# Performance work log

Measured on AMD Instinct MI355X. Metric: run time of the kernel, lower is better.

Reference implementation:

```python
import jax, jax.numpy as jnp
import numpy as np

B, S, D = 2, 2048, 4096
H, KV = 32, 8
HD = D // H  # 128
REP = H // KV  # 4
THETA = 10000.0


def _rope(x, cos, sin):
    # x: [B, S, N, HD]; cos/sin: [S, HD//2]
    xs = x.reshape(*x.shape[:-1], HD // 2, 2)
    x0, x1 = xs[..., 0], xs[..., 1]
    c = cos[None, :, None, :]
    s = sin[None, :, None, :]
    r0 = x0 * c - x1 * s
    r1 = x0 * s + x1 * c
    return jnp.stack([r0, r1], axis=-1).reshape(x.shape)


def setup_inputs() -> dict:
    key = jax.random.key(0)
    kx, kq, kk, kv, ko = jax.random.split(key, 5)
    x = jax.random.normal(kx, (B, S, D), dtype=jnp.float32)
    # faithful rope frequencies (precompute_freqs_cis equivalent)
    inv_freq = 1.0 / (THETA ** (np.arange(0, HD, 2, dtype=np.float32) / HD))
    freqs = np.outer(np.arange(S, dtype=np.float32), inv_freq)  # [S, HD//2]
    freqs_cos = jnp.asarray(np.cos(freqs))
    freqs_sin = jnp.asarray(np.sin(freqs))
    std = 0.02
    wq = jax.random.normal(kq, (H * HD, D), dtype=jnp.float32) * std
    wk = jax.random.normal(kk, (KV * HD, D), dtype=jnp.float32) * std
    wv = jax.random.normal(kv, (KV * HD, D), dtype=jnp.float32) * std
    wo = jax.random.normal(ko, (D, H * HD), dtype=jnp.float32) * std
    return {"x": x, "freqs_cos": freqs_cos, "freqs_sin": freqs_sin,
            "wq": wq, "wk": wk, "wv": wv, "wo": wo}


def reference(x, freqs_cos, freqs_sin, wq, wk, wv, wo):
    bs, seqlen, _ = x.shape
    q = (x @ wq.T).reshape(bs, seqlen, H, HD)
    k = (x @ wk.T).reshape(bs, seqlen, KV, HD)
    v = (x @ wv.T).reshape(bs, seqlen, KV, HD)
    q = _rope(q, freqs_cos, freqs_sin)
    k = _rope(k, freqs_cos, freqs_sin)
    # GQA: group query heads by kv head instead of materializing repeat_kv
    qg = q.reshape(bs, seqlen, KV, REP, HD)
    scale = 1.0 / jnp.sqrt(jnp.float32(HD))
    scores = jnp.einsum("bqgrd,bkgd->bgrqk", qg, k) * scale  # [B,KV,REP,S,S]
    causal = jnp.tril(jnp.ones((seqlen, seqlen), dtype=bool))
    scores = jnp.where(causal, scores, -jnp.inf)
    probs = jax.nn.softmax(scores, axis=-1)
    out = jnp.einsum("bgrqk,bkgd->bqgrd", probs, v)  # [B,S,KV,REP,HD]
    out = out.reshape(bs, seqlen, H * HD)
    return out @ wo.T
```

## Files before the change

### kernel.cpp

```cpp
#include <hip/hip_runtime.h>
#include <hip/hip_bf16.h>

#define BB 2
#define SS 2048
#define DD 4096
#define HH 32
#define KVH 8
#define HDD 128

using bf16 = __hip_bfloat16;
typedef __attribute__((ext_vector_type(8))) __bf16 bf16x8;
typedef __attribute__((ext_vector_type(4))) float f32x4;

#define GLOAD16(gp, lp) __builtin_amdgcn_global_load_lds(                     \
    (const __attribute__((address_space(1))) void*)(gp),                      \
    (__attribute__((address_space(3))) void*)(lp), 16, 0, 0)

__global__ __launch_bounds__(256) void cast_kernel(
    const float* __restrict__ s, bf16* __restrict__ d, int n4) {
  int i = blockIdx.x * blockDim.x + threadIdx.x;
  if (i >= n4) return;
  float4 v = ((const float4*)s)[i];
  bf16 a0 = __float2bfloat16(v.x), a1 = __float2bfloat16(v.y);
  bf16 a2 = __float2bfloat16(v.z), a3 = __float2bfloat16(v.w);
  ushort4 u;
  u.x = reinterpret_cast<unsigned short&>(a0);
  u.y = reinterpret_cast<unsigned short&>(a1);
  u.z = reinterpret_cast<unsigned short&>(a2);
  u.w = reinterpret_cast<unsigned short&>(a3);
  ((ushort4*)d)[i] = u;
}

__global__ __launch_bounds__(256) void rope_kernel(
    bf16* __restrict__ qb, bf16* __restrict__ kb,
    const float* __restrict__ fc, const float* __restrict__ fs) {
  int idx = blockIdx.x * blockDim.x + threadIdx.x;
  const int QP = BB * SS * HH * (HDD / 2);
  const int KP = BB * SS * KVH * (HDD / 2);
  bf16* p;
  int s, i;
  if (idx < QP) {
    int hr = idx >> 6;
    s = (hr >> 5) & (SS - 1);
    i = idx & 63;
    p = qb + ((size_t)hr << 7) + (i << 1);
  } else {
    int j = idx - QP;
    if (j >= KP) return;
    int hr = j >> 6;
    s = (hr >> 3) & (SS - 1);
    i = j & 63;
    p = kb + ((size_t)hr << 7) + (i << 1);
  }
  float c = fc[s * 64 + i], sn = fs[s * 64 + i];
  float x0 = __bfloat162float(p[0]), x1 = __bfloat162float(p[1]);
  p[0] = __float2bfloat16(x0 * c - x1 * sn);
  p[1] = __float2bfloat16(x0 * sn + x1 * c);
}

template <int MODE>
__global__ __launch_bounds__(256, 2) void gemm_bt(
    const bf16* __restrict__ A, const bf16* __restrict__ Bm,
    void* __restrict__ C, int M, int N, int K) {
  __shared__ __attribute__((aligned(16))) bf16 As[128 * 64];
  __shared__ __attribute__((aligned(16))) bf16 Bs[128 * 64];
  const int m0 = blockIdx.y * 128, n0 = blockIdx.x * 128;
  const int t = threadIdx.x;
  const int lane = t & 63, w = t >> 6;
  const int wm = (w >> 1) * 64, wn = (w & 1) * 64;
  const int lr = lane & 15, quad = lane >> 4;

  const int srow = t >> 3;
  const int scol8 = ((t & 7) ^ (srow & 7)) * 8;
  const bf16* aSrc = A + (size_t)(m0 + srow) * K + scol8;
  const bf16* bSrc = Bm + (size_t)(n0 + srow) * K + scol8;
  bf16* aDst = As + t * 8;
  bf16* bDst = Bs + t * 8;

  const int sl[2] = {((0 * 4 + quad) ^ (lr & 7)) * 8, ((1 * 4 + quad) ^ (lr & 7)) * 8};

  f32x4 acc[4][4];
#pragma unroll
  for (int i = 0; i < 4; i++)
#pragma unroll
    for (int j = 0; j < 4; j++) acc[i][j] = (f32x4)0.0f;

  for (int k0 = 0; k0 < K; k0 += 64) {
#pragma unroll
    for (int i = 0; i < 4; i++) {
      GLOAD16(aSrc + i * 32 * K, aDst + i * 2048);
      GLOAD16(bSrc + i * 32 * K, bDst + i * 2048);
    }
    __syncthreads();
#pragma unroll
    for (int kk = 0; kk < 2; kk++) {
      bf16x8 af[4], bfv[4];
#pragma unroll
      for (int i = 0; i < 4; i++)
        af[i] = *(const bf16x8*)(As + (wm + i * 16 + lr) * 64 + sl[kk]);
#pragma unroll
      for (int j = 0; j < 4; j++)
        bfv[j] = *(const bf16x8*)(Bs + (wn + j * 16 + lr) * 64 + sl[kk]);
#pragma unroll
      for (int i = 0; i < 4; i++)
#pragma unroll
        for (int j = 0; j < 4; j++)
          acc[i][j] = __builtin_amdgcn_mfma_f32_16x16x32_bf16(af[i], bfv[j], acc[i][j], 0, 0, 0);
    }
    __syncthreads();
    aSrc += 64;
    bSrc += 64;
  }

#pragma unroll
  for (int i = 0; i < 4; i++)
#pragma unroll
    for (int j = 0; j < 4; j++)
#pragma unroll
      for (int r = 0; r < 4; r++) {
        int row = m0 + wm + i * 16 + quad * 4 + r;
        int col = n0 + wn + j * 16 + lr;
        float v = acc[i][j][r];
        if (MODE == 0) {
          ((bf16*)C)[(size_t)row * N + col] = __float2bfloat16(v);
        } else if (MODE == 1) {
          ((float*)C)[(size_t)row * N + col] = v;
        } else {
          int bb = row >> 11, s = row & (SS - 1);
          int kv = col >> 7, d = col & (HDD - 1);
          ((bf16*)C)[((size_t)(bb * KVH + kv) * HDD + d) * SS + s] = __float2bfloat16(v);
        }
      }
}

__global__ __launch_bounds__(256, 2) void flash_kernel(
    const bf16* __restrict__ q, const bf16* __restrict__ k,
    const bf16* __restrict__ vt, bf16* __restrict__ out) {
  __shared__ __attribute__((aligned(16))) bf16 Ks[64 * 128];
  __shared__ __attribute__((aligned(16))) bf16 Vs[128 * 64];
  __shared__ __attribute__((aligned(16))) bf16 Ps[128 * 72];
  const int qt = gridDim.x - 1 - blockIdx.x;
  const int h = blockIdx.y, b = blockIdx.z;
  const int kv = h >> 2;
  const int t = threadIdx.x;
  const int lane = t & 63, w = t >> 6;
  const int lr = lane & 15, quad = lane >> 4;
  const int q0 = qt * 128;
  const int wr = w * 32;

  bf16x8 qf[2][4];
#pragma unroll
  for (int mf = 0; mf < 2; mf++) {
    const bf16* qp =
        q + ((size_t)(b * SS + q0 + wr + mf * 16 + lr) * HH + h) * HDD + quad * 8;
#pragma unroll
    for (int c = 0; c < 4; c++) qf[mf][c] = *(const bf16x8*)(qp + c * 32);
  }
  const float scale = 0.08838834764831845f;
#pragma unroll
  for (int mf = 0; mf < 2; mf++)
#pragma unroll
    for (int c = 0; c < 4; c++)
#pragma unroll
      for (int j = 0; j < 8; j++)
        qf[mf][c][j] = (__bf16)((float)qf[mf][c][j] * scale);

  f32x4 oa[2][8];
#pragma unroll
  for (int mf = 0; mf < 2; mf++)
#pragma unroll
    for (int i = 0; i < 8; i++) oa[mf][i] = (f32x4)0.0f;
  float m_i[8], l_i[8];
#pragma unroll
  for (int r = 0; r < 8; r++) { m_i[r] = -1e30f; l_i[r] = 0.f; }

  const int krow = t >> 4;
  const int kcol8 = ((t & 15) ^ (krow & 15)) * 8;
  const bf16* kSrc0 = k + ((size_t)(b * SS + krow) * KVH + kv) * HDD + kcol8;
  const int vrow = t >> 3;
  const int vcol8 = ((t & 7) ^ (vrow & 7)) * 8;
  const bf16* vSrc0 = vt + ((size_t)(b * KVH + kv) * HDD + vrow) * SS + vcol8;
  bf16* kDst = Ks + t * 8;
  bf16* vDst = Vs + t * 8;

  const int slV[2] = {((0 * 4 + quad) ^ (lr & 7)) * 8, ((1 * 4 + quad) ^ (lr & 7)) * 8};

  const int nkt = 2 * qt + 2;
  for (int kt = 0; kt < nkt; kt++) {
    const int kt0 = kt * 64;
    const bf16* kSrc = kSrc0 + (size_t)kt0 * (KVH * HDD);
    const bf16* vSrc = vSrc0 + kt0;
#pragma unroll
    for (int i = 0; i < 4; i++) {
      GLOAD16(kSrc + i * 16 * KVH * HDD, kDst + i * 2048);
      GLOAD16(vSrc + i * 32 * SS, vDst + i * 2048);
    }
    __syncthreads();

    f32x4 sc[2][4];
#pragma unroll
    for (int mf = 0; mf < 2; mf++)
#pragma unroll
      for (int ni = 0; ni < 4; ni++) sc[mf][ni] = (f32x4)0.0f;
#pragma unroll
    for (int c = 0; c < 4; c++) {
      bf16x8 kf[4];
#pragma unroll
      for (int ni = 0; ni < 4; ni++)
        kf[ni] = *(const bf16x8*)(Ks + (ni * 16 + lr) * 128 + (((c * 4 + quad) ^ lr) * 8));
#pragma unroll
      for (int mf = 0; mf < 2; mf++)
#pragma unroll
        for (int ni = 0; ni < 4; ni++)
          sc[mf][ni] = __builtin_amdgcn_mfma_f32_16x16x32_bf16(qf[mf][c], kf[ni], sc[mf][ni], 0, 0, 0);
    }

    if (kt0 + 63 > q0 + wr) {
#pragma unroll
      for (int mf = 0; mf < 2; mf++)
#pragma unroll
        for (int ni = 0; ni < 4; ni++)
#pragma unroll
          for (int r = 0; r < 4; r++) {
            int kidx = kt0 + ni * 16 + lr;
            int qidx = q0 + wr + mf * 16 + quad * 4 + r;
            if (kidx > qidx) sc[mf][ni][r] = -1e30f;
          }
    }

    float mx[8];
#pragma unroll
    for (int r = 0; r < 8; r++) mx[r] = -1e30f;
#pragma unroll
    for (int mf = 0; mf < 2; mf++)
#pragma unroll
      for (int ni = 0; ni < 4; ni++)
#pragma unroll
        for (int r = 0; r < 4; r++)
          mx[mf * 4 + r] = fmaxf(mx[mf * 4 + r], sc[mf][ni][r]);
#pragma unroll
    for (int off = 1; off < 16; off <<= 1)
#pragma unroll
      for (int r = 0; r < 8; r++) mx[r] = fmaxf(mx[r], __shfl_xor(mx[r], off));

    float alpha[8], rs[8];
#pragma unroll
    for (int r = 0; r < 8; r++) {
      float mn = fmaxf(m_i[r], mx[r]);
      alpha[r] = __expf(m_i[r] - mn);
      m_i[r] = mn;
      rs[r] = 0.f;
    }
#pragma unroll
    for (int mf = 0; mf < 2; mf++)
#pragma unroll
      for (int ni = 0; ni < 4; ni++)
#pragma unroll
        for (int r = 0; r < 4; r++) {
          float p = __expf(sc[mf][ni][r] - m_i[mf * 4 + r]);
          sc[mf][ni][r] = p;
          rs[mf * 4 + r] += p;
        }
#pragma unroll
    for (int off = 1; off < 16; off <<= 1)
#pragma unroll
      for (int r = 0; r < 8; r++) rs[r] += __shfl_xor(rs[r], off);
#pragma unroll
    for (int r = 0; r < 8; r++) l_i[r] = l_i[r] * alpha[r] + rs[r];
#pragma unroll
    for (int mf = 0; mf < 2; mf++)
#pragma unroll
      for (int ni = 0; ni < 8; ni++)
#pragma unroll
        for (int r = 0; r < 4; r++) oa[mf][ni][r] *= alpha[mf * 4 + r];

#pragma unroll
    for (int mf = 0; mf < 2; mf++)
#pragma unroll
      for (int ni = 0; ni < 4; ni++)
#pragma unroll
        for (int r = 0; r < 4; r++)
          Ps[(wr + mf * 16 + quad * 4 + r) * 72 + ni * 16 + lr] =
              __float2bfloat16(sc[mf][ni][r]);

#pragma unroll
    for (int kk = 0; kk < 2; kk++) {
      bf16x8 pf[2];
#pragma unroll
      for (int mf = 0; mf < 2; mf++)
        pf[mf] = *(const bf16x8*)(Ps + (wr + mf * 16 + lr) * 72 + kk * 32 + quad * 8);
#pragma unroll
      for (int ni = 0; ni < 8; ni++) {
        bf16x8 vf = *(const bf16x8*)(Vs + (ni * 16 + lr) * 64 + slV[kk]);
#pragma unroll
        for (int mf = 0; mf < 2; mf++)
          oa[mf][ni] = __builtin_amdgcn_mfma_f32_16x16x32_bf16(pf[mf], vf, oa[mf][ni], 0, 0, 0);
      }
    }
    __syncthreads();
  }

#pragma unroll
  for (int mf = 0; mf < 2; mf++)
#pragma unroll
    for (int r = 0; r < 4; r++) {
      float inv = 1.0f / l_i[mf * 4 + r];
      int srow = q0 + wr + mf * 16 + quad * 4 + r;
#pragma unroll
      for (int ni = 0; ni < 8; ni++) {
        int col = ni * 16 + lr;
        out[(size_t)(b * SS + srow) * DD + h * HDD + col] =
            __float2bfloat16(oa[mf][ni][r] * inv);
      }
    }
}

extern "C" void kernel_launch(void* const* d_in, const int* in_sizes, int n_in,
                              void* d_out, int out_size, void* d_ws, size_t ws_size,
                              hipStream_t stream) {
  (void)in_sizes; (void)n_in; (void)out_size; (void)ws_size;
  const float* x  = (const float*)d_in[0];
  const float* fc = (const float*)d_in[1];
  const float* fs = (const float*)d_in[2];
  const float* wq = (const float*)d_in[3];
  const float* wk = (const float*)d_in[4];
  const float* wv = (const float*)d_in[5];
  const float* wo = (const float*)d_in[6];

  char* ws = (char*)d_ws;
  bf16* xb   = (bf16*)(ws);
  bf16* W    = (bf16*)(ws + (size_t)33554432);
  bf16* qb   = (bf16*)(ws + (size_t)67108864);
  bf16* kb   = (bf16*)(ws + (size_t)100663296);
  bf16* vtb  = (bf16*)(ws + (size_t)109051904);
  bf16* attn = xb;

  const int NX  = BB * SS * DD;
  const int NW  = DD * DD;
  const int NWK = KVH * HDD * DD;

  cast_kernel<<<NX / 1024, 256, 0, stream>>>(x, xb, NX / 4);
  cast_kernel<<<NW / 1024, 256, 0, stream>>>(wq, W, NW / 4);
  gemm_bt<0><<<dim3(32, 32), 256, 0, stream>>>(xb, W, qb, BB * SS, DD, DD);
  cast_kernel<<<NWK / 1024, 256, 0, stream>>>(wk, W, NWK / 4);
  gemm_bt<0><<<dim3(8, 32), 256, 0, stream>>>(xb, W, kb, BB * SS, KVH * HDD, DD);
  cast_kernel<<<NWK / 1024, 256, 0, stream>>>(wv, W, NWK / 4);
  gemm_bt<2><<<dim3(8, 32), 256, 0, stream>>>(xb, W, vtb, BB * SS, KVH * HDD, DD);
  rope_kernel<<<(BB * SS * (HH + KVH) * 64) / 256, 256, 0, stream>>>(qb, kb, fc, fs);
  flash_kernel<<<dim3(SS / 128, HH, BB), 256, 0, stream>>>(qb, kb, vtb, attn);
  cast_kernel<<<NW / 1024, 256, 0, stream>>>(wo, W, NW / 4);
  gemm_bt<1><<<dim3(32, 32), 256, 0, stream>>>(attn, W, (float*)d_out, BB * SS, DD, DD);
}
```

Measured before the change: 858.5 us.

## Fuse K/V projections, fold softmax scale into RoPE, transpose score MFMA

The K and V projection GEMMs become one launch over a concatenated 2048-column weight, with the epilogue routing K columns row-major and V columns transposed. The softmax scale and log2(e) are folded into the Q RoPE pass, so the flash kernel drops its per-load Q scaling and uses exp2. The score MFMA operands are swapped so each lane holds one query row, which cuts the row max and sum reductions to two cross-lane shuffles and lets P be written to LDS as packed 8-byte stores. In exchange, the per-row alpha and l factors must be broadcast with extra shuffles, and Q is rounded to bf16 after scaling.

```diff
diff --git a/kernel.cpp b/kernel.cpp
--- a/kernel.cpp
+++ b/kernel.cpp
@@ -15,6 +15,12 @@
 #define GLOAD16(gp, lp) __builtin_amdgcn_global_load_lds(                     \
     (const __attribute__((address_space(1))) void*)(gp),                      \
     (__attribute__((address_space(3))) void*)(lp), 16, 0, 0)
+
+__device__ inline unsigned pack_bf16_2(float a, float b) {
+  unsigned short ua = __bfloat16_as_ushort(__float2bfloat16(a));
+  unsigned short ub = __bfloat16_as_ushort(__float2bfloat16(b));
+  return (unsigned)ua | ((unsigned)ub << 16);
+}
 
 __global__ __launch_bounds__(256) void cast_kernel(
     const float* __restrict__ s, bf16* __restrict__ d, int n4) {
@@ -34,16 +40,19 @@
 __global__ __launch_bounds__(256) void rope_kernel(
     bf16* __restrict__ qb, bf16* __restrict__ kb,
     const float* __restrict__ fc, const float* __restrict__ fs) {
+  const float QS = 0.08838834764831845f * 1.4426950408889634f;
   int idx = blockIdx.x * blockDim.x + threadIdx.x;
   const int QP = BB * SS * HH * (HDD / 2);
   const int KP = BB * SS * KVH * (HDD / 2);
   bf16* p;
   int s, i;
+  float g;
   if (idx < QP) {
     int hr = idx >> 6;
     s = (hr >> 5) & (SS - 1);
     i = idx & 63;
     p = qb + ((size_t)hr << 7) + (i << 1);
+    g = QS;
   } else {
     int j = idx - QP;
     if (j >= KP) return;
@@ -51,17 +60,18 @@
     s = (hr >> 3) & (SS - 1);
     i = j & 63;
     p = kb + ((size_t)hr << 7) + (i << 1);
+    g = 1.0f;
   }
   float c = fc[s * 64 + i], sn = fs[s * 64 + i];
   float x0 = __bfloat162float(p[0]), x1 = __bfloat162float(p[1]);
-  p[0] = __float2bfloat16(x0 * c - x1 * sn);
-  p[1] = __float2bfloat16(x0 * sn + x1 * c);
+  p[0] = __float2bfloat16((x0 * c - x1 * sn) * g);
+  p[1] = __float2bfloat16((x0 * sn + x1 * c) * g);
 }
 
 template <int MODE>
 __global__ __launch_bounds__(256, 2) void gemm_bt(
     const bf16* __restrict__ A, const bf16* __restrict__ Bm,
-    void* __restrict__ C, int M, int N, int K) {
+    void* __restrict__ C, void* __restrict__ C2, int M, int N, int K) {
   __shared__ __attribute__((aligned(16))) bf16 As[128 * 64];
   __shared__ __attribute__((aligned(16))) bf16 Bs[128 * 64];
   const int m0 = blockIdx.y * 128, n0 = blockIdx.x * 128;
@@ -126,9 +136,15 @@
         } else if (MODE == 1) {
           ((float*)C)[(size_t)row * N + col] = v;
         } else {
-          int bb = row >> 11, s = row & (SS - 1);
-          int kv = col >> 7, d = col & (HDD - 1);
-          ((bf16*)C)[((size_t)(bb * KVH + kv) * HDD + d) * SS + s] = __float2bfloat16(v);
+          if (n0 < 1024) {
+            ((bf16*)C)[(size_t)row * 1024 + col] = __float2bfloat16(v);
+          } else {
+            int c2 = col - 1024;
+            int kv = c2 >> 7, d = c2 & (HDD - 1);
+            int bb = row >> 11, s = row & (SS - 1);
+            ((bf16*)C2)[((size_t)(bb * KVH + kv) * HDD + d) * SS + s] =
+                __float2bfloat16(v);
+          }
         }
       }
 }
@@ -156,23 +172,13 @@
 #pragma unroll
     for (int c = 0; c < 4; c++) qf[mf][c] = *(const bf16x8*)(qp + c * 32);
   }
-  const float scale = 0.08838834764831845f;
+
+  f32x4 oa[2][8];
 #pragma unroll
   for (int mf = 0; mf < 2; mf++)
 #pragma unroll
-    for (int c = 0; c < 4; c++)
-#pragma unroll
-      for (int j = 0; j < 8; j++)
-        qf[mf][c][j] = (__bf16)((float)qf[mf][c][j] * scale);
-
-  f32x4 oa[2][8];
-#pragma unroll
-  for (int mf = 0; mf < 2; mf++)
-#pragma unroll
     for (int i = 0; i < 8; i++) oa[mf][i] = (f32x4)0.0f;
-  float m_i[8], l_i[8];
-#pragma unroll
-  for (int r = 0; r < 8; r++) { m_i[r] = -1e30f; l_i[r] = 0.f; }
+  float m_i[2] = {-1e30f, -1e30f}, l_i[2] = {0.f, 0.f};
 
   const int krow = t >> 4;
   const int kcol8 = ((t & 15) ^ (krow & 15)) * 8;
@@ -184,6 +190,8 @@
   bf16* vDst = Vs + t * 8;
 
   const int slV[2] = {((0 * 4 + quad) ^ (lr & 7)) * 8, ((1 * 4 + quad) ^ (lr & 7)) * 8};
+  bf16* psw0 = Ps + (wr + lr) * 72;
+  bf16* psw1 = Ps + (wr + 16 + lr) * 72;
 
   const int nkt = 2 * qt + 2;
   for (int kt = 0; kt < nkt; kt++) {
@@ -197,11 +205,11 @@
     }
     __syncthreads();
 
-    f32x4 sc[2][4];
+    f32x4 st[2][4];
 #pragma unroll
     for (int mf = 0; mf < 2; mf++)
 #pragma unroll
-      for (int ni = 0; ni < 4; ni++) sc[mf][ni] = (f32x4)0.0f;
+      for (int ni = 0; ni < 4; ni++) st[mf][ni] = (f32x4)0.0f;
 #pragma unroll
     for (int c = 0; c < 4; c++) {
       bf16x8 kf[4];
@@ -212,83 +220,76 @@
       for (int mf = 0; mf < 2; mf++)
 #pragma unroll
         for (int ni = 0; ni < 4; ni++)
-          sc[mf][ni] = __builtin_amdgcn_mfma_f32_16x16x32_bf16(qf[mf][c], kf[ni], sc[mf][ni], 0, 0, 0);
+          st[mf][ni] = __builtin_amdgcn_mfma_f32_16x16x32_bf16(kf[ni], qf[mf][c], st[mf][ni], 0, 0, 0);
     }
 
     if (kt0 + 63 > q0 + wr) {
 #pragma unroll
-      for (int mf = 0; mf < 2; mf++)
+      for (int mf = 0; mf < 2; mf++) {
+        int qidx = q0 + wr + mf * 16 + lr;
 #pragma unroll
         for (int ni = 0; ni < 4; ni++)
 #pragma unroll
           for (int r = 0; r < 4; r++) {
-            int kidx = kt0 + ni * 16 + lr;
-            int qidx = q0 + wr + mf * 16 + quad * 4 + r;
-            if (kidx > qidx) sc[mf][ni][r] = -1e30f;
+            int kidx = kt0 + ni * 16 + quad * 4 + r;
+            if (kidx > qidx) st[mf][ni][r] = -1e30f;
           }
-    }
-
-    float mx[8];
-#pragma unroll
-    for (int r = 0; r < 8; r++) mx[r] = -1e30f;
-#pragma unroll
-    for (int mf = 0; mf < 2; mf++)
+      }
+    }
+
+    float alpha[2], rs[2];
+#pragma unroll
+    for (int mf = 0; mf < 2; mf++) {
+      float mx = st[mf][0][0];
 #pragma unroll
       for (int ni = 0; ni < 4; ni++)
 #pragma unroll
-        for (int r = 0; r < 4; r++)
-          mx[mf * 4 + r] = fmaxf(mx[mf * 4 + r], sc[mf][ni][r]);
-#pragma unroll
-    for (int off = 1; off < 16; off <<= 1)
-#pragma unroll
-      for (int r = 0; r < 8; r++) mx[r] = fmaxf(mx[r], __shfl_xor(mx[r], off));
-
-    float alpha[8], rs[8];
-#pragma unroll
-    for (int r = 0; r < 8; r++) {
-      float mn = fmaxf(m_i[r], mx[r]);
-      alpha[r] = __expf(m_i[r] - mn);
-      m_i[r] = mn;
-      rs[r] = 0.f;
-    }
-#pragma unroll
-    for (int mf = 0; mf < 2; mf++)
+        for (int r = 0; r < 4; r++) mx = fmaxf(mx, st[mf][ni][r]);
+      mx = fmaxf(mx, __shfl_xor(mx, 16));
+      mx = fmaxf(mx, __shfl_xor(mx, 32));
+      float mn = fmaxf(m_i[mf], mx);
+      alpha[mf] = __builtin_amdgcn_exp2f(m_i[mf] - mn);
+      m_i[mf] = mn;
+      float s = 0.f;
 #pragma unroll
       for (int ni = 0; ni < 4; ni++)
 #pragma unroll
         for (int r = 0; r < 4; r++) {
-          float p = __expf(sc[mf][ni][r] - m_i[mf * 4 + r]);
-          sc[mf][ni][r] = p;
-          rs[mf * 4 + r] += p;
+          float p = __builtin_amdgcn_exp2f(st[mf][ni][r] - mn);
+          st[mf][ni][r] = p;
+          s += p;
         }
-#pragma unroll
-    for (int off = 1; off < 16; off <<= 1)
-#pragma unroll
-      for (int r = 0; r < 8; r++) rs[r] += __shfl_xor(rs[r], off);
-#pragma unroll
-    for (int r = 0; r < 8; r++) l_i[r] = l_i[r] * alpha[r] + rs[r];
-#pragma unroll
-    for (int mf = 0; mf < 2; mf++)
-#pragma unroll
-      for (int ni = 0; ni < 8; ni++)
-#pragma unroll
-        for (int r = 0; r < 4; r++) oa[mf][ni][r] *= alpha[mf * 4 + r];
-
-#pragma unroll
-    for (int mf = 0; mf < 2; mf++)
-#pragma unroll
-      for (int ni = 0; ni < 4; ni++)
-#pragma unroll
-        for (int r = 0; r < 4; r++)
-          Ps[(wr + mf * 16 + quad * 4 + r) * 72 + ni * 16 + lr] =
-              __float2bfloat16(sc[mf][ni][r]);
+      s += __shfl_xor(s, 16);
+      s += __shfl_xor(s, 32);
+      rs[mf] = s;
+      l_i[mf] = l_i[mf] * alpha[mf] + s;
+    }
+
+#pragma unroll
+    for (int ni = 0; ni < 4; ni++) {
+      uint2 u0, u1;
+      u0.x = pack_bf16_2(st[0][ni][0], st[0][ni][1]);
+      u0.y = pack_bf16_2(st[0][ni][2], st[0][ni][3]);
+      u1.x = pack_bf16_2(st[1][ni][0], st[1][ni][1]);
+      u1.y = pack_bf16_2(st[1][ni][2], st[1][ni][3]);
+      *(uint2*)(psw0 + ni * 16 + quad * 4) = u0;
+      *(uint2*)(psw1 + ni * 16 + quad * 4) = u1;
+    }
+
+#pragma unroll
+    for (int mf = 0; mf < 2; mf++) {
+      f32x4 av;
+#pragma unroll
+      for (int r = 0; r < 4; r++) av[r] = __shfl(alpha[mf], quad * 4 + r);
+#pragma unroll
+      for (int ni = 0; ni < 8; ni++) oa[mf][ni] *= av;
+    }
 
 #pragma unroll
     for (int kk = 0; kk < 2; kk++) {
       bf16x8 pf[2];
-#pragma unroll
-      for (int mf = 0; mf < 2; mf++)
-        pf[mf] = *(const bf16x8*)(Ps + (wr + mf * 16 + lr) * 72 + kk * 32 + quad * 8);
+      pf[0] = *(const bf16x8*)(psw0 + kk * 32 + quad * 8);
+      pf[1] = *(const bf16x8*)(psw1 + kk * 32 + quad * 8);
 #pragma unroll
       for (int ni = 0; ni < 8; ni++) {
         bf16x8 vf = *(const bf16x8*)(Vs + (ni * 16 + lr) * 64 + slV[kk]);
@@ -301,18 +302,21 @@
   }
 
 #pragma unroll
-  for (int mf = 0; mf < 2; mf++)
+  for (int mf = 0; mf < 2; mf++) {
+    f32x4 linv;
+#pragma unroll
+    for (int r = 0; r < 4; r++) linv[r] = 1.0f / __shfl(l_i[mf], quad * 4 + r);
 #pragma unroll
     for (int r = 0; r < 4; r++) {
-      float inv = 1.0f / l_i[mf * 4 + r];
       int srow = q0 + wr + mf * 16 + quad * 4 + r;
 #pragma unroll
       for (int ni = 0; ni < 8; ni++) {
         int col = ni * 16 + lr;
         out[(size_t)(b * SS + srow) * DD + h * HDD + col] =
-            __float2bfloat16(oa[mf][ni][r] * inv);
+            __float2bfloat16(oa[mf][ni][r] * linv[r]);
       }
     }
+  }
 }
 
 extern "C" void kernel_launch(void* const* d_in, const int* in_sizes, int n_in,
@@ -341,13 +345,12 @@
 
   cast_kernel<<<NX / 1024, 256, 0, stream>>>(x, xb, NX / 4);
   cast_kernel<<<NW / 1024, 256, 0, stream>>>(wq, W, NW / 4);
-  gemm_bt<0><<<dim3(32, 32), 256, 0, stream>>>(xb, W, qb, BB * SS, DD, DD);
+  gemm_bt<0><<<dim3(32, 32), 256, 0, stream>>>(xb, W, qb, nullptr, BB * SS, DD, DD);
   cast_kernel<<<NWK / 1024, 256, 0, stream>>>(wk, W, NWK / 4);
-  gemm_bt<0><<<dim3(8, 32), 256, 0, stream>>>(xb, W, kb, BB * SS, KVH * HDD, DD);
-  cast_kernel<<<NWK / 1024, 256, 0, stream>>>(wv, W, NWK / 4);
-  gemm_bt<2><<<dim3(8, 32), 256, 0, stream>>>(xb, W, vtb, BB * SS, KVH * HDD, DD);
+  cast_kernel<<<NWK / 1024, 256, 0, stream>>>(wv, W + 4194304, NWK / 4);
+  gemm_bt<2><<<dim3(16, 32), 256, 0, stream>>>(xb, W, kb, vtb, BB * SS, 2048, DD);
   rope_kernel<<<(BB * SS * (HH + KVH) * 64) / 256, 256, 0, stream>>>(qb, kb, fc, fs);
   flash_kernel<<<dim3(SS / 128, HH, BB), 256, 0, stream>>>(qb, kb, vtb, attn);
   cast_kernel<<<NW / 1024, 256, 0, stream>>>(wo, W, NW / 4);
-  gemm_bt<1><<<dim3(32, 32), 256, 0, stream>>>(attn, W, (float*)d_out, BB * SS, DD, DD);
-}
+  gemm_bt<1><<<dim3(32, 32), 256, 0, stream>>>(attn, W, (float*)d_out, nullptr, BB * SS, DD, DD);
+}
```

After: 795.2 us. 7.4% less time.
